# Performance work log

Measured on AMD Instinct MI355X. Metric: run time of the kernel, lower is better.

## Reference

```python
import jax, jax.numpy as jnp
import numpy as np

N = 100_000      # nodes
E = 1_600_000    # edges (avg degree 16)
IN, H, OUT = 960, 192, 3
NB = 6           # block_num


def setup_inputs() -> dict:
    key = jax.random.key(0)
    ks = jax.random.split(key, 14)
    s = 0.05  # weight init scale
    x = jax.random.normal(ks[0], (N, IN), jnp.float32)
    src = jax.random.randint(ks[1], (E,), 0, N, jnp.int32)
    dst = jax.random.randint(ks[2], (E,), 0, N, jnp.int32)
    # normalized adjacency values (like D^-1 A entries)
    ew = jax.random.uniform(ks[3], (E,), jnp.float32) / 16.0
    w1 = jax.random.normal(ks[4], (IN, H), jnp.float32) * s
    l1 = jax.random.normal(ks[5], (IN, H), jnp.float32) * s
    b1 = jnp.zeros((H,), jnp.float32)
    wb = jax.random.normal(ks[6], (2 * NB, H, H), jnp.float32) * s
    lb = jax.random.normal(ks[7], (2 * NB, H, H), jnp.float32) * s
    bb = jnp.zeros((2 * NB, H), jnp.float32)
    w2 = jax.random.normal(ks[8], (H, OUT), jnp.float32) * s
    l2 = jax.random.normal(ks[9], (H, OUT), jnp.float32) * s
    b2 = jnp.zeros((OUT,), jnp.float32)
    return dict(x=x, src=src, dst=dst, ew=ew, w1=w1, l1=l1, b1=b1,
                wb=wb, lb=lb, bb=bb, w2=w2, l2=l2, b2=b2)


def reference(x, src, dst, ew, w1, l1, b1, wb, lb, bb, w2, l2, b2):
    def gcn(h, w, lw, b):
        # GraphConvolution: spmm(adj, h @ w) + h @ loop_w + b
        sup = h @ w                                   # [N, F_out]
        msg = sup[src] * ew[:, None]                  # gather + weight  [E, F_out]
        agg = jax.ops.segment_sum(msg, dst, num_segments=N)
        return agg + h @ lw + b

    h = gcn(x, w1, l1, b1)                            # conv1: in_dim -> hidden
    for i in range(NB):                               # GResBlocks
        a = gcn(h, wb[2 * i], lb[2 * i], bb[2 * i])
        a = gcn(a, wb[2 * i + 1], lb[2 * i + 1], bb[2 * i + 1])
        h = (h + a) * 0.5                             # residual scaling
    x_cat = h
    x_out = gcn(x_cat, w2, l2, b2)                    # conv2: hidden -> out_dim
    return (x_out, x_cat)
```

## Files before the change

kernel.cpp:

```cpp
#include <hip/hip_runtime.h>

typedef __attribute__((ext_vector_type(8))) short short8;
typedef __attribute__((ext_vector_type(4))) float f32x4;
typedef __attribute__((ext_vector_type(4))) int int4v;
typedef __attribute__((ext_vector_type(2))) unsigned int u32x2;

__device__ __forceinline__ float bf2f(unsigned short u) {
  return __uint_as_float(((unsigned)u) << 16);
}
__device__ __forceinline__ unsigned short f2bf(float f) {
  unsigned u = __float_as_uint(f);
  return (unsigned short)((u + 0x7FFFu + ((u >> 16) & 1u)) >> 16);
}

#define GLB_CAST(p) ((const __attribute__((address_space(1))) void*)(p))
#define LDS_CAST(p) ((__attribute__((address_space(3))) void*)(p))

__global__ void count_kernel(const int* __restrict__ dst, int* __restrict__ cnt, int E) {
  int e = blockIdx.x * blockDim.x + threadIdx.x;
  if (e < E) atomicAdd(&cnt[dst[e] + 1], 1);
}

__global__ __launch_bounds__(256) void scan_bsum_kernel(const int* __restrict__ cnt,
                                                        int* __restrict__ bsum, int n) {
  __shared__ int buf[256];
  int tid = threadIdx.x;
  int j0 = blockIdx.x * 1024 + tid * 4;
  int s = 0;
#pragma unroll
  for (int k = 0; k < 4; k++) {
    int j = j0 + k;
    if (j < n) s += cnt[j];
  }
  buf[tid] = s;
  __syncthreads();
  for (int off = 128; off > 0; off >>= 1) {
    if (tid < off) buf[tid] += buf[tid + off];
    __syncthreads();
  }
  if (tid == 0) bsum[blockIdx.x] = buf[0];
}

__global__ __launch_bounds__(256) void scan_small_kernel(const int* __restrict__ bsum,
                                                         int* __restrict__ boff, int nb) {
  __shared__ int buf[2][256];
  int tid = threadIdx.x;
  int C = (nb + 255) >> 8;
  int start = tid * C;
  int end = start + C; if (end > nb) end = nb;
  int s = 0;
  for (int j = start; j < end; j++) s += bsum[j];
  buf[0][tid] = s;
  __syncthreads();
  int pin = 0;
  for (int off = 1; off < 256; off <<= 1) {
    int v = buf[pin][tid];
    if (tid >= off) v += buf[pin][tid - off];
    buf[pin ^ 1][tid] = v;
    pin ^= 1;
    __syncthreads();
  }
  int run = (tid == 0) ? 0 : buf[pin][tid - 1];
  for (int j = start; j < end; j++) {
    boff[j] = run;
    run += bsum[j];
  }
}

__global__ __launch_bounds__(256) void scan_final_kernel(const int* __restrict__ cnt,
                                                         const int* __restrict__ boff,
                                                         int* __restrict__ rowptr,
                                                         int* __restrict__ cur,
                                                         int n, int nrows) {
  __shared__ int buf[2][256];
  int tid = threadIdx.x;
  int j0 = blockIdx.x * 1024 + tid * 4;
  int v[4];
  int s = 0;
#pragma unroll
  for (int k = 0; k < 4; k++) {
    int j = j0 + k;
    v[k] = (j < n) ? cnt[j] : 0;
    s += v[k];
  }
  buf[0][tid] = s;
  __syncthreads();
  int pin = 0;
  for (int off = 1; off < 256; off <<= 1) {
    int t = buf[pin][tid];
    if (tid >= off) t += buf[pin][tid - off];
    buf[pin ^ 1][tid] = t;
    pin ^= 1;
    __syncthreads();
  }
  int run = boff[blockIdx.x] + ((tid == 0) ? 0 : buf[pin][tid - 1]);
#pragma unroll
  for (int k = 0; k < 4; k++) {
    int j = j0 + k;
    if (j < n) {
      run += v[k];
      rowptr[j] = run;
      if (j < nrows) cur[j] = run;
    }
  }
}

__global__ void fill_kernel(const int* __restrict__ src, const int* __restrict__ dst,
                            const float* __restrict__ ew,
                            int* __restrict__ cur, int2* __restrict__ s_edge, int E) {
  int e = blockIdx.x * blockDim.x + threadIdx.x;
  if (e >= E) return;
  int r = dst[e];
  int pos = atomicAdd(&cur[r], 1);
  s_edge[pos] = make_int2(src[e], __float_as_int(ew[e]));
}

__global__ void prep_w_kernel(const float* __restrict__ w1,
                              const float* __restrict__ l1,
                              const float* __restrict__ wb,
                              const float* __restrict__ lb,
                              unsigned short* __restrict__ Wt1,
                              unsigned short* __restrict__ Wcatb) {
  int tid = blockIdx.x * blockDim.x + threadIdx.x;
  const int n1 = 384 * 960;
  const int nc = 12 * 192 * 384;
  if (tid < n1) {
    int c = tid / 960, k = tid % 960;
    Wt1[tid] = f2bf((c < 192) ? w1[k * 192 + c] : l1[k * 192 + (c - 192)]);
  } else if (tid < n1 + nc) {
    int u = tid - n1;
    int i = u / (192 * 384);
    int r = u % (192 * 384);
    int c = r / 384, k = r % 384;
    Wcatb[u] = f2bf((k < 192) ? wb[((size_t)i * 192 + k) * 192 + c]
                              : lb[((size_t)i * 192 + (k - 192)) * 192 + c]);
  }
}

__device__ __forceinline__ short8 cvt_pair(f32x4 a, f32x4 b) {
  short8 r;
  r[0] = (short)f2bf(a[0]); r[1] = (short)f2bf(a[1]);
  r[2] = (short)f2bf(a[2]); r[3] = (short)f2bf(a[3]);
  r[4] = (short)f2bf(b[0]); r[5] = (short)f2bf(b[1]);
  r[6] = (short)f2bf(b[2]); r[7] = (short)f2bf(b[3]);
  return r;
}

__global__ __launch_bounds__(512) void gemm_f32_kernel(const float* __restrict__ A,
                                                       const unsigned short* __restrict__ Wt,
                                                       unsigned short* __restrict__ out,
                                                       int nrows, int K) {
  __shared__ char lds_raw[40960];

  int tid = threadIdx.x;
  int lane = tid & 63;
  int w = tid >> 6;
  int rg = w >> 1, ch = w & 1;
  int row0blk = blockIdx.x * 256;
  int row0 = row0blk + rg * 64;
  int l15 = lane & 15, lq = lane >> 4;

  f32x4 acc[12][4];
#pragma unroll
  for (int cf = 0; cf < 12; cf++)
#pragma unroll
    for (int rf = 0; rf < 4; rf++) acc[cf][rf] = (f32x4)(0.0f);

  int tiles = K / 32;
  for (int tile = 0; tile < tiles; ++tile) {
    __syncthreads();
#pragma unroll
    for (int it = 0; it < 3; ++it) {
      int slot = it * 512 + tid;
      int q = slot / 384, c = slot - q * 384;
      const unsigned short* g = Wt + (size_t)c * K + tile * 32 + q * 8;
      __builtin_amdgcn_global_load_lds(GLB_CAST(g), LDS_CAST(lds_raw + 16384 + slot * 16), 16, 0, 0);
    }
#pragma unroll
    for (int it = 0; it < 2; ++it) {
      int slot = it * 512 + tid;
      int c = slot >> 8, row = slot & 255;
      int grow = row0blk + row;
      if (grow > nrows - 1) grow = nrows - 1;
      const float* g = A + (size_t)grow * K + tile * 32 + c * 8;
      f32x4 a0 = *reinterpret_cast<const f32x4*>(g);
      f32x4 a1 = *reinterpret_cast<const f32x4*>(g + 4);
      *reinterpret_cast<short8*>(lds_raw + slot * 16) = cvt_pair(a0, a1);
    }
    __syncthreads();

    short8 af[4];
#pragma unroll
    for (int rf = 0; rf < 4; rf++)
      af[rf] = *reinterpret_cast<const short8*>(
          lds_raw + lq * 4096 + (rg * 64 + rf * 16 + l15) * 16);
#pragma unroll
    for (int cf = 0; cf < 12; cf++) {
      const short8 bf = *reinterpret_cast<const short8*>(
          lds_raw + 16384 + (lq * 384 + ch * 192 + cf * 16 + l15) * 16);
#pragma unroll
      for (int rf = 0; rf < 4; rf++)
        acc[cf][rf] = __builtin_amdgcn_mfma_f32_16x16x32_bf16(bf, af[rf], acc[cf][rf], 0, 0, 0);
    }
  }

#pragma unroll
  for (int rf = 0; rf < 4; rf++) {
    int row = row0 + rf * 16 + l15;
    if (row >= nrows) continue;
    unsigned short* orow = out + (size_t)row * 384 + ch * 192 + lq * 4;
#pragma unroll
    for (int cf = 0; cf < 12; cf++) {
      u32x2 pv;
      pv[0] = (unsigned)f2bf(acc[cf][rf][0]) | ((unsigned)f2bf(acc[cf][rf][1]) << 16);
      pv[1] = (unsigned)f2bf(acc[cf][rf][2]) | ((unsigned)f2bf(acc[cf][rf][3]) << 16);
      *reinterpret_cast<u32x2*>(orow + cf * 16) = pv;
    }
  }
}

__global__ __launch_bounds__(256) void gemm_cat_kernel(const unsigned short* __restrict__ A1,
                                                       const unsigned short* __restrict__ A2,
                                                       const unsigned short* __restrict__ Wcat,
                                                       const float* __restrict__ bias,
                                                       const unsigned short* __restrict__ hprev,
                                                       unsigned short* __restrict__ out,
                                                       int nrows) {
  __shared__ char lds[28672];

  int tid = threadIdx.x;
  int lane = tid & 63;
  int rg = tid >> 6;
  int row0blk = blockIdx.x * 256;
  int l15 = lane & 15, lq = lane >> 4;

  f32x4 acc[12][4];
#pragma unroll
  for (int cf = 0; cf < 12; cf++)
#pragma unroll
    for (int rf = 0; rf < 4; rf++) acc[cf][rf] = (f32x4)(0.0f);

  for (int tile = 0; tile < 12; ++tile) {
    __syncthreads();
#pragma unroll
    for (int it = 0; it < 3; ++it) {
      int slot = it * 256 + tid;
      int q = slot / 192, c = slot - q * 192;
      const unsigned short* g = Wcat + (size_t)c * 384 + tile * 32 + q * 8;
      __builtin_amdgcn_global_load_lds(GLB_CAST(g), LDS_CAST(lds + 16384 + slot * 16), 16, 0, 0);
    }
    {
      const unsigned short* arr = (tile < 6) ? A1 : A2;
      int koff = (tile < 6 ? tile : tile - 6) * 32;
#pragma unroll
      for (int it = 0; it < 4; ++it) {
        int slot = it * 256 + tid;
        int q = slot >> 8, row = slot & 255;
        int grow = row0blk + row;
        if (grow > nrows - 1) grow = nrows - 1;
        const unsigned short* g = arr + (size_t)grow * 192 + koff + q * 8;
        __builtin_amdgcn_global_load_lds(GLB_CAST(g), LDS_CAST(lds + slot * 16), 16, 0, 0);
      }
    }
    __syncthreads();

    short8 af[4];
#pragma unroll
    for (int rf = 0; rf < 4; rf++)
      af[rf] = *reinterpret_cast<const short8*>(
          lds + (lq * 256 + rg * 64 + rf * 16 + l15) * 16);
#pragma unroll
    for (int cf = 0; cf < 12; cf++) {
      const short8 bf = *reinterpret_cast<const short8*>(
          lds + 16384 + (lq * 192 + cf * 16 + l15) * 16);
#pragma unroll
      for (int rf = 0; rf < 4; rf++)
        acc[cf][rf] = __builtin_amdgcn_mfma_f32_16x16x32_bf16(bf, af[rf], acc[cf][rf], 0, 0, 0);
    }
  }

#pragma unroll
  for (int rf = 0; rf < 4; rf++) {
    int row = row0blk + rg * 64 + rf * 16 + l15;
    if (row >= nrows) continue;
    unsigned short* orow = out + (size_t)row * 192 + lq * 4;
#pragma unroll
    for (int cf = 0; cf < 12; cf++) {
      int col = cf * 16 + lq * 4;
      f32x4 bv = *reinterpret_cast<const f32x4*>(bias + col);
      float r[4];
#pragma unroll
      for (int j = 0; j < 4; j++) r[j] = acc[cf][rf][j] + bv[j];
      if (hprev) {
        u32x2 hp = *reinterpret_cast<const u32x2*>(&hprev[(size_t)row * 192 + col]);
        r[0] = 0.5f * (bf2f((unsigned short)(hp[0] & 0xFFFF)) + r[0]);
        r[1] = 0.5f * (bf2f((unsigned short)(hp[0] >> 16)) + r[1]);
        r[2] = 0.5f * (bf2f((unsigned short)(hp[1] & 0xFFFF)) + r[2]);
        r[3] = 0.5f * (bf2f((unsigned short)(hp[1] >> 16)) + r[3]);
      }
      u32x2 pv;
      pv[0] = (unsigned)f2bf(r[0]) | ((unsigned)f2bf(r[1]) << 16);
      pv[1] = (unsigned)f2bf(r[2]) | ((unsigned)f2bf(r[3]) << 16);
      *reinterpret_cast<u32x2*>(orow + cf * 16) = pv;
    }
  }
}

__global__ __launch_bounds__(256) void spmm_t_kernel(const unsigned short* __restrict__ t,
                                                     const int* __restrict__ rowptr,
                                                     const int2* __restrict__ s_edge,
                                                     const float* __restrict__ bias,
                                                     unsigned short* __restrict__ out16,
                                                     int n) {
  int tid = blockIdx.x * blockDim.x + threadIdx.x;
  int node = tid >> 3;
  int sub = tid & 7;
  if (node >= n) return;
  int co = sub * 8;

  float acc[3][8];
#pragma unroll
  for (int q = 0; q < 3; q++)
#pragma unroll
    for (int j = 0; j < 8; j++) acc[q][j] = 0.0f;

  int e0 = rowptr[node], e1 = rowptr[node + 1];
  int ne = e1 - e0;
  int base = 0;
  for (; base + 8 <= ne; base += 8) {
    int2 rec = s_edge[e0 + base + sub];
#pragma unroll
    for (int half = 0; half < 2; half++) {
      short8 v[4][3];
      float wgt[4];
#pragma unroll
      for (int k = 0; k < 4; k++) {
        int kk = half * 4 + k;
        int sn = __shfl(rec.x, kk, 8);
        wgt[k] = __int_as_float(__shfl(rec.y, kk, 8));
        const unsigned short* row = t + (size_t)sn * 384;
#pragma unroll
        for (int q = 0; q < 3; q++)
          v[k][q] = *reinterpret_cast<const short8*>(row + q * 64 + co);
      }
#pragma unroll
      for (int k = 0; k < 4; k++)
#pragma unroll
        for (int q = 0; q < 3; q++)
#pragma unroll
          for (int j = 0; j < 8; j++)
            acc[q][j] += wgt[k] * bf2f((unsigned short)v[k][q][j]);
    }
  }
  for (; base < ne; base++) {
    int2 rec = s_edge[e0 + base];
    float wgt = __int_as_float(rec.y);
    const unsigned short* row = t + (size_t)rec.x * 384;
#pragma unroll
    for (int q = 0; q < 3; q++) {
      short8 v = *reinterpret_cast<const short8*>(row + q * 64 + co);
#pragma unroll
      for (int j = 0; j < 8; j++) acc[q][j] += wgt * bf2f((unsigned short)v[j]);
    }
  }

  const unsigned short* hlrow = t + (size_t)node * 384 + 192;
#pragma unroll
  for (int q = 0; q < 3; q++) {
    short8 hlv = *reinterpret_cast<const short8*>(hlrow + q * 64 + co);
    unsigned short o16[8];
#pragma unroll
    for (int j = 0; j < 8; j++)
      o16[j] = f2bf(acc[q][j] + bf2f((unsigned short)hlv[j]) + bias[q * 64 + co + j]);
    *reinterpret_cast<int4v*>(&out16[(size_t)node * 192 + q * 64 + co]) =
        *reinterpret_cast<const int4v*>(o16);
  }
}

__global__ __launch_bounds__(256) void spmm_g_kernel(const unsigned short* __restrict__ h,
                                                     const int* __restrict__ rowptr,
                                                     const int2* __restrict__ s_edge,
                                                     unsigned short* __restrict__ g16,
                                                     int n) {
  int tid = blockIdx.x * blockDim.x + threadIdx.x;
  int node = tid >> 3;
  int sub = tid & 7;
  if (node >= n) return;
  int co = sub * 8;

  float acc[3][8];
#pragma unroll
  for (int q = 0; q < 3; q++)
#pragma unroll
    for (int j = 0; j < 8; j++) acc[q][j] = 0.0f;

  int e0 = rowptr[node], e1 = rowptr[node + 1];
  int ne = e1 - e0;
  int base = 0;
  for (; base + 8 <= ne; base += 8) {
    int2 rec = s_edge[e0 + base + sub];
#pragma unroll
    for (int half = 0; half < 2; half++) {
      short8 v[4][3];
      float wgt[4];
#pragma unroll
      for (int k = 0; k < 4; k++) {
        int kk = half * 4 + k;
        int sn = __shfl(rec.x, kk, 8);
        wgt[k] = __int_as_float(__shfl(rec.y, kk, 8));
        const unsigned short* row = h + (size_t)sn * 192;
#pragma unroll
        for (int q = 0; q < 3; q++)
          v[k][q] = *reinterpret_cast<const short8*>(row + q * 64 + co);
      }
#pragma unroll
      for (int k = 0; k < 4; k++)
#pragma unroll
        for (int q = 0; q < 3; q++)
#pragma unroll
          for (int j = 0; j < 8; j++)
            acc[q][j] += wgt[k] * bf2f((unsigned short)v[k][q][j]);
    }
  }
  for (; base < ne; base++) {
    int2 rec = s_edge[e0 + base];
    float wgt = __int_as_float(rec.y);
    const unsigned short* row = h + (size_t)rec.x * 192;
#pragma unroll
    for (int q = 0; q < 3; q++) {
      short8 v = *reinterpret_cast<const short8*>(row + q * 64 + co);
#pragma unroll
      for (int j = 0; j < 8; j++) acc[q][j] += wgt * bf2f((unsigned short)v[j]);
    }
  }

#pragma unroll
  for (int q = 0; q < 3; q++) {
    unsigned short o16[8];
#pragma unroll
    for (int j = 0; j < 8; j++) o16[j] = f2bf(acc[q][j]);
    *reinterpret_cast<int4v*>(&g16[(size_t)node * 192 + q * 64 + co]) =
        *reinterpret_cast<const int4v*>(o16);
  }
}

__global__ __launch_bounds__(256) void cvt_kernel(const unsigned short* __restrict__ h16,
                                                  float* __restrict__ h32, int n8) {
  int i = blockIdx.x * blockDim.x + threadIdx.x;
  if (i >= n8) return;
  short8 v = *reinterpret_cast<const short8*>(&h16[(size_t)i * 8]);
  f32x4 lo, hi;
#pragma unroll
  for (int j = 0; j < 4; j++) {
    lo[j] = bf2f((unsigned short)v[j]);
    hi[j] = bf2f((unsigned short)v[4 + j]);
  }
  *reinterpret_cast<f32x4*>(&h32[(size_t)i * 8]) = lo;
  *reinterpret_cast<f32x4*>(&h32[(size_t)i * 8 + 4]) = hi;
}

__global__ __launch_bounds__(256) void conv2a_kernel(const unsigned short* __restrict__ h,
                                                     const float* __restrict__ w2,
                                                     const float* __restrict__ l2,
                                                     const float* __restrict__ b2,
                                                     float* __restrict__ sup2,
                                                     float* __restrict__ hl2, int n) {
  int wid = (blockIdx.x * blockDim.x + threadIdx.x) >> 6;
  int lane = threadIdx.x & 63;
  if (wid >= n) return;
  float sa[3] = {0.f, 0.f, 0.f}, sl[3] = {0.f, 0.f, 0.f};
  for (int k = lane; k < 192; k += 64) {
    float hv = bf2f(h[(size_t)wid * 192 + k]);
#pragma unroll
    for (int j = 0; j < 3; j++) {
      sa[j] += hv * w2[k * 3 + j];
      sl[j] += hv * l2[k * 3 + j];
    }
  }
#pragma unroll
  for (int j = 0; j < 3; j++) {
    for (int off = 32; off > 0; off >>= 1) {
      sa[j] += __shfl_down(sa[j], off);
      sl[j] += __shfl_down(sl[j], off);
    }
  }
  if (lane == 0) {
#pragma unroll
    for (int j = 0; j < 3; j++) {
      sup2[(size_t)wid * 3 + j] = sa[j];
      hl2[(size_t)wid * 3 + j] = sl[j] + b2[j];
    }
  }
}

__global__ __launch_bounds__(256) void conv2b_kernel(const int* __restrict__ rowptr,
                                                     const int2* __restrict__ s_edge,
                                                     const float* __restrict__ sup2,
                                                     const float* __restrict__ hl2,
                                                     float* __restrict__ out, int n) {
  int node = blockIdx.x * blockDim.x + threadIdx.x;
  if (node >= n) return;
  float acc[3] = {0.f, 0.f, 0.f};
  int e0 = rowptr[node], e1 = rowptr[node + 1];
  for (int e = e0; e < e1; e++) {
    int2 rec = s_edge[e];
    float wgt = __int_as_float(rec.y);
#pragma unroll
    for (int j = 0; j < 3; j++) acc[j] += wgt * sup2[(size_t)rec.x * 3 + j];
  }
#pragma unroll
  for (int j = 0; j < 3; j++)
    out[(size_t)node * 3 + j] = acc[j] + hl2[(size_t)node * 3 + j];
}

extern "C" void kernel_launch(void* const* d_in, const int* in_sizes, int n_in,
                              void* d_out, int out_size, void* d_ws, size_t ws_size,
                              hipStream_t stream) {
  const float* x  = (const float*)d_in[0];
  const int* src  = (const int*)d_in[1];
  const int* dst  = (const int*)d_in[2];
  const float* ew = (const float*)d_in[3];
  const float* w1 = (const float*)d_in[4];
  const float* l1 = (const float*)d_in[5];
  const float* b1 = (const float*)d_in[6];
  const float* wb = (const float*)d_in[7];
  const float* lb = (const float*)d_in[8];
  const float* bb = (const float*)d_in[9];
  const float* w2 = (const float*)d_in[10];
  const float* l2 = (const float*)d_in[11];
  const float* b2 = (const float*)d_in[12];
  float* out = (float*)d_out;

  const int N = in_sizes[0] / 960;
  const int E = in_sizes[1];

  float* h32 = out + (size_t)N * 3;

  char* p = (char*)d_ws;
  auto alloc = [&](size_t bytes) {
    char* q = p;
    p += (bytes + 255) & ~(size_t)255;
    return q;
  };
  unsigned short* Wt1   = (unsigned short*)alloc((size_t)384 * 960 * 2);
  unsigned short* Wcatb = (unsigned short*)alloc((size_t)12 * 192 * 384 * 2);
  unsigned short* t     = (unsigned short*)alloc((size_t)N * 384 * 2);
  unsigned short* h16a  = (unsigned short*)alloc((size_t)N * 192 * 2);
  unsigned short* h16b  = (unsigned short*)alloc((size_t)N * 192 * 2);
  int* rowptr = (int*)alloc((size_t)(N + 1) * 4);
  int* cur    = (int*)alloc((size_t)N * 4);
  int* cnt    = (int*)alloc((size_t)(N + 1) * 4);
  int* bsum   = (int*)alloc((size_t)1024 * 4);
  int* boff   = (int*)alloc((size_t)1024 * 4);
  int2* s_edge = (int2*)alloc((size_t)E * 8);
  float* sup2 = (float*)alloc((size_t)N * 3 * 4);
  float* hl2  = (float*)alloc((size_t)N * 3 * 4);
  if ((size_t)(p - (char*)d_ws) > ws_size) return;

  unsigned short* g16 = t;
  unsigned short* a16 = t + (size_t)N * 192;

  const int nScan = N + 1;
  const int nBlk = (nScan + 1023) / 1024;

  hipMemsetAsync(cnt, 0, (size_t)(N + 1) * 4, stream);
  count_kernel<<<(E + 255) / 256, 256, 0, stream>>>(dst, cnt, E);
  scan_bsum_kernel<<<nBlk, 256, 0, stream>>>(cnt, bsum, nScan);
  scan_small_kernel<<<1, 256, 0, stream>>>(bsum, boff, nBlk);
  scan_final_kernel<<<nBlk, 256, 0, stream>>>(cnt, boff, rowptr, cur, nScan, N);
  fill_kernel<<<(E + 255) / 256, 256, 0, stream>>>(src, dst, ew, cur, s_edge, E);
  {
    int total = 384 * 960 + 12 * 192 * 384;
    prep_w_kernel<<<(total + 255) / 256, 256, 0, stream>>>(w1, l1, wb, lb, Wt1, Wcatb);
  }

  int gBlocks = (N + 255) / 256;
  int sBlocks = (N * 8 + 255) / 256;

  gemm_f32_kernel<<<gBlocks, 512, 0, stream>>>(x, Wt1, t, N, 960);
  spmm_t_kernel<<<sBlocks, 256, 0, stream>>>(t, rowptr, s_edge, b1, h16a, N);

  unsigned short* hcur = h16a;
  unsigned short* hnxt = h16b;
  for (int i = 0; i < 12; i += 2) {
    spmm_g_kernel<<<sBlocks, 256, 0, stream>>>(hcur, rowptr, s_edge, g16, N);
    gemm_cat_kernel<<<gBlocks, 256, 0, stream>>>(
        g16, hcur, Wcatb + (size_t)i * 192 * 384, bb + (size_t)i * 192,
        (const unsigned short*)nullptr, a16, N);
    spmm_g_kernel<<<sBlocks, 256, 0, stream>>>(a16, rowptr, s_edge, g16, N);
    gemm_cat_kernel<<<gBlocks, 256, 0, stream>>>(
        g16, a16, Wcatb + (size_t)(i + 1) * 192 * 384, bb + (size_t)(i + 1) * 192,
        hcur, hnxt, N);
    unsigned short* tmp = hcur; hcur = hnxt; hnxt = tmp;
  }

  cvt_kernel<<<(N * 24 + 255) / 256, 256, 0, stream>>>(hcur, h32, N * 24);

  conv2a_kernel<<<(N + 3) / 4, 256, 0, stream>>>(hcur, w2, l2, b2, sup2, hl2, N);
  conv2b_kernel<<<(N + 255) / 256, 256, 0, stream>>>(rowptr, s_edge, sup2, hl2, out, N);
}
```

Baseline: 2.653 ms.

## Fuse SpMM aggregation into the residual-block GEMM through LDS

Each residual-block GCN layer now runs as one kernel instead of two. The kernel first gathers neighbour rows for 128 nodes and writes the aggregated bf16 tile into LDS. It then runs the concatenated GEMM against the weights, with double-buffered weight and self-feature tiles. This removes the global write and reread of the intermediate g16 buffer and half the launches. In exchange each block uses 72KB of dynamic LDS, has fewer rows per block (128 vs 256), and the weights are reloaded more often.

```diff
diff --git a/kernel.cpp b/kernel.cpp
--- a/kernel.cpp
+++ b/kernel.cpp
@@ -219,78 +219,218 @@
   }
 }
 
-__global__ __launch_bounds__(256) void gemm_cat_kernel(const unsigned short* __restrict__ A1,
-                                                       const unsigned short* __restrict__ A2,
-                                                       const unsigned short* __restrict__ Wcat,
-                                                       const float* __restrict__ bias,
-                                                       const unsigned short* __restrict__ hprev,
-                                                       unsigned short* __restrict__ out,
-                                                       int nrows) {
-  __shared__ char lds[28672];
+__global__ __launch_bounds__(256) void spmm_t_kernel(const unsigned short* __restrict__ t,
+                                                     const int* __restrict__ rowptr,
+                                                     const int2* __restrict__ s_edge,
+                                                     const float* __restrict__ bias,
+                                                     unsigned short* __restrict__ out16,
+                                                     int n) {
+  int tid = blockIdx.x * blockDim.x + threadIdx.x;
+  int node = tid >> 3;
+  int sub = tid & 7;
+  if (node >= n) return;
+  int co = sub * 8;
+
+  float acc[3][8];
+#pragma unroll
+  for (int q = 0; q < 3; q++)
+#pragma unroll
+    for (int j = 0; j < 8; j++) acc[q][j] = 0.0f;
+
+  int e0 = rowptr[node], e1 = rowptr[node + 1];
+  int ne = e1 - e0;
+  int base = 0;
+  for (; base + 8 <= ne; base += 8) {
+    int2 rec = s_edge[e0 + base + sub];
+#pragma unroll
+    for (int half = 0; half < 2; half++) {
+      short8 v[4][3];
+      float wgt[4];
+#pragma unroll
+      for (int k = 0; k < 4; k++) {
+        int kk = half * 4 + k;
+        int sn = __shfl(rec.x, kk, 8);
+        wgt[k] = __int_as_float(__shfl(rec.y, kk, 8));
+        const unsigned short* row = t + (size_t)sn * 384;
+#pragma unroll
+        for (int q = 0; q < 3; q++)
+          v[k][q] = *reinterpret_cast<const short8*>(row + q * 64 + co);
+      }
+#pragma unroll
+      for (int k = 0; k < 4; k++)
+#pragma unroll
+        for (int q = 0; q < 3; q++)
+#pragma unroll
+          for (int j = 0; j < 8; j++)
+            acc[q][j] += wgt[k] * bf2f((unsigned short)v[k][q][j]);
+    }
+  }
+  for (; base < ne; base++) {
+    int2 rec = s_edge[e0 + base];
+    float wgt = __int_as_float(rec.y);
+    const unsigned short* row = t + (size_t)rec.x * 384;
+#pragma unroll
+    for (int q = 0; q < 3; q++) {
+      short8 v = *reinterpret_cast<const short8*>(row + q * 64 + co);
+#pragma unroll
+      for (int j = 0; j < 8; j++) acc[q][j] += wgt * bf2f((unsigned short)v[j]);
+    }
+  }
+
+  const unsigned short* hlrow = t + (size_t)node * 384 + 192;
+#pragma unroll
+  for (int q = 0; q < 3; q++) {
+    short8 hlv = *reinterpret_cast<const short8*>(hlrow + q * 64 + co);
+    unsigned short o16[8];
+#pragma unroll
+    for (int j = 0; j < 8; j++)
+      o16[j] = f2bf(acc[q][j] + bf2f((unsigned short)hlv[j]) + bias[q * 64 + co + j]);
+    *reinterpret_cast<int4v*>(&out16[(size_t)node * 192 + q * 64 + co]) =
+        *reinterpret_cast<const int4v*>(o16);
+  }
+}
+
+__global__ __launch_bounds__(512) void fused_res_kernel(const unsigned short* __restrict__ h,
+                                                        const int* __restrict__ rowptr,
+                                                        const int2* __restrict__ s_edge,
+                                                        const unsigned short* __restrict__ Wcat,
+                                                        const float* __restrict__ bias,
+                                                        const unsigned short* __restrict__ hprev,
+                                                        unsigned short* __restrict__ outp,
+                                                        int n) {
+  extern __shared__ char lds[];
+  const int BOFF = 49152;
 
   int tid = threadIdx.x;
   int lane = tid & 63;
+  int row0 = blockIdx.x * 128;
+
+  {
+    int nloc = tid >> 2;
+    int sub = tid & 3;
+    int grow = row0 + nloc;
+    if (grow > n - 1) grow = n - 1;
+    float acc[6][8];
+#pragma unroll
+    for (int jq = 0; jq < 6; jq++)
+#pragma unroll
+      for (int j = 0; j < 8; j++) acc[jq][j] = 0.0f;
+
+    int e0 = rowptr[grow], e1 = rowptr[grow + 1];
+    int ne = e1 - e0;
+    int base = 0;
+    for (; base + 4 <= ne; base += 4) {
+      int2 rec = s_edge[e0 + base + sub];
+#pragma unroll
+      for (int kp = 0; kp < 2; kp++) {
+        short8 v[2][6];
+        float wg[2];
+#pragma unroll
+        for (int k = 0; k < 2; k++) {
+          int kk = kp * 2 + k;
+          int sn = __shfl(rec.x, kk, 4);
+          wg[k] = __int_as_float(__shfl(rec.y, kk, 4));
+          const unsigned short* rowp = h + (size_t)sn * 192;
+#pragma unroll
+          for (int jq = 0; jq < 6; jq++)
+            v[k][jq] = *reinterpret_cast<const short8*>(rowp + (jq * 4 + sub) * 8);
+        }
+#pragma unroll
+        for (int k = 0; k < 2; k++)
+#pragma unroll
+          for (int jq = 0; jq < 6; jq++)
+#pragma unroll
+            for (int j = 0; j < 8; j++)
+              acc[jq][j] += wg[k] * bf2f((unsigned short)v[k][jq][j]);
+      }
+    }
+    for (; base < ne; base++) {
+      int2 rec = s_edge[e0 + base];
+      float wg = __int_as_float(rec.y);
+      const unsigned short* rowp = h + (size_t)rec.x * 192;
+#pragma unroll
+      for (int jq = 0; jq < 6; jq++) {
+        short8 v = *reinterpret_cast<const short8*>(rowp + (jq * 4 + sub) * 8);
+#pragma unroll
+        for (int j = 0; j < 8; j++) acc[jq][j] += wg * bf2f((unsigned short)v[j]);
+      }
+    }
+#pragma unroll
+    for (int jq = 0; jq < 6; jq++) {
+      int q = jq * 4 + sub;
+      unsigned short o[8];
+#pragma unroll
+      for (int j = 0; j < 8; j++) o[j] = f2bf(acc[jq][j]);
+      *reinterpret_cast<int4v*>(lds + (q * 128 + nloc) * 16) =
+          *reinterpret_cast<const int4v*>(o);
+    }
+  }
+
+  auto stageB = [&](int t, int buf) {
+    {
+      int slot = tid;
+      int q = slot / 192, c = slot - q * 192;
+      const unsigned short* g = Wcat + (size_t)c * 384 + t * 32 + q * 8;
+      __builtin_amdgcn_global_load_lds(GLB_CAST(g),
+                                       LDS_CAST(lds + BOFF + buf * 12288 + slot * 16), 16, 0, 0);
+    }
+    if (tid < 256) {
+      int slot = 512 + tid;
+      int q = slot / 192, c = slot - q * 192;
+      const unsigned short* g = Wcat + (size_t)c * 384 + t * 32 + q * 8;
+      __builtin_amdgcn_global_load_lds(GLB_CAST(g),
+                                       LDS_CAST(lds + BOFF + buf * 12288 + slot * 16), 16, 0, 0);
+    }
+  };
+
+  stageB(0, 0);
+  __syncthreads();
+
   int rg = tid >> 6;
-  int row0blk = blockIdx.x * 256;
   int l15 = lane & 15, lq = lane >> 4;
-
-  f32x4 acc[12][4];
-#pragma unroll
-  for (int cf = 0; cf < 12; cf++)
-#pragma unroll
-    for (int rf = 0; rf < 4; rf++) acc[cf][rf] = (f32x4)(0.0f);
-
-  for (int tile = 0; tile < 12; ++tile) {
-    __syncthreads();
-#pragma unroll
-    for (int it = 0; it < 3; ++it) {
-      int slot = it * 256 + tid;
-      int q = slot / 192, c = slot - q * 192;
-      const unsigned short* g = Wcat + (size_t)c * 384 + tile * 32 + q * 8;
-      __builtin_amdgcn_global_load_lds(GLB_CAST(g), LDS_CAST(lds + 16384 + slot * 16), 16, 0, 0);
-    }
-    {
-      const unsigned short* arr = (tile < 6) ? A1 : A2;
-      int koff = (tile < 6 ? tile : tile - 6) * 32;
-#pragma unroll
-      for (int it = 0; it < 4; ++it) {
-        int slot = it * 256 + tid;
-        int q = slot >> 8, row = slot & 255;
-        int grow = row0blk + row;
-        if (grow > nrows - 1) grow = nrows - 1;
-        const unsigned short* g = arr + (size_t)grow * 192 + koff + q * 8;
-        __builtin_amdgcn_global_load_lds(GLB_CAST(g), LDS_CAST(lds + slot * 16), 16, 0, 0);
+  f32x4 acc[12];
+#pragma unroll
+  for (int cf = 0; cf < 12; cf++) acc[cf] = (f32x4)(0.0f);
+
+  for (int t = 0; t < 12; ++t) {
+    if (t + 1 < 12) {
+      stageB(t + 1, (t + 1) & 1);
+      if (t + 1 >= 6) {
+        int slot = tid;
+        int q = slot >> 7, row = slot & 127;
+        int grow = row0 + row;
+        if (grow > n - 1) grow = n - 1;
+        const unsigned short* g = h + (size_t)grow * 192 + (t + 1 - 6) * 32 + q * 8;
+        __builtin_amdgcn_global_load_lds(GLB_CAST(g),
+                                         LDS_CAST(lds + ((t + 1) & 1) * 8192 + slot * 16), 16, 0, 0);
       }
     }
-    __syncthreads();
-
-    short8 af[4];
-#pragma unroll
-    for (int rf = 0; rf < 4; rf++)
-      af[rf] = *reinterpret_cast<const short8*>(
-          lds + (lq * 256 + rg * 64 + rf * 16 + l15) * 16);
+
+    short8 af;
+    if (t < 6)
+      af = *reinterpret_cast<const short8*>(lds + ((t * 4 + lq) * 128 + rg * 16 + l15) * 16);
+    else
+      af = *reinterpret_cast<const short8*>(lds + (t & 1) * 8192 + (lq * 128 + rg * 16 + l15) * 16);
+
 #pragma unroll
     for (int cf = 0; cf < 12; cf++) {
       const short8 bf = *reinterpret_cast<const short8*>(
-          lds + 16384 + (lq * 192 + cf * 16 + l15) * 16);
-#pragma unroll
-      for (int rf = 0; rf < 4; rf++)
-        acc[cf][rf] = __builtin_amdgcn_mfma_f32_16x16x32_bf16(bf, af[rf], acc[cf][rf], 0, 0, 0);
-    }
-  }
-
-#pragma unroll
-  for (int rf = 0; rf < 4; rf++) {
-    int row = row0blk + rg * 64 + rf * 16 + l15;
-    if (row >= nrows) continue;
-    unsigned short* orow = out + (size_t)row * 192 + lq * 4;
+          lds + BOFF + (t & 1) * 12288 + (lq * 192 + cf * 16 + l15) * 16);
+      acc[cf] = __builtin_amdgcn_mfma_f32_16x16x32_bf16(bf, af, acc[cf], 0, 0, 0);
+    }
+    __syncthreads();
+  }
+
+  int row = row0 + rg * 16 + l15;
+  if (row < n) {
+    unsigned short* orow = outp + (size_t)row * 192 + lq * 4;
 #pragma unroll
     for (int cf = 0; cf < 12; cf++) {
       int col = cf * 16 + lq * 4;
       f32x4 bv = *reinterpret_cast<const f32x4*>(bias + col);
       float r[4];
 #pragma unroll
-      for (int j = 0; j < 4; j++) r[j] = acc[cf][rf][j] + bv[j];
+      for (int j = 0; j < 4; j++) r[j] = acc[cf][j] + bv[j];
       if (hprev) {
         u32x2 hp = *reinterpret_cast<const u32x2*>(&hprev[(size_t)row * 192 + col]);
         r[0] = 0.5f * (bf2f((unsigned short)(hp[0] & 0xFFFF)) + r[0]);
@@ -303,144 +443,6 @@
       pv[1] = (unsigned)f2bf(r[2]) | ((unsigned)f2bf(r[3]) << 16);
       *reinterpret_cast<u32x2*>(orow + cf * 16) = pv;
     }
-  }
-}
-
-__global__ __launch_bounds__(256) void spmm_t_kernel(const unsigned short* __restrict__ t,
-                                                     const int* __restrict__ rowptr,
-                                                     const int2* __restrict__ s_edge,
-                                                     const float* __restrict__ bias,
-                                                     unsigned short* __restrict__ out16,
-                                                     int n) {
-  int tid = blockIdx.x * blockDim.x + threadIdx.x;
-  int node = tid >> 3;
-  int sub = tid & 7;
-  if (node >= n) return;
-  int co = sub * 8;
-
-  float acc[3][8];
-#pragma unroll
-  for (int q = 0; q < 3; q++)
-#pragma unroll
-    for (int j = 0; j < 8; j++) acc[q][j] = 0.0f;
-
-  int e0 = rowptr[node], e1 = rowptr[node + 1];
-  int ne = e1 - e0;
-  int base = 0;
-  for (; base + 8 <= ne; base += 8) {
-    int2 rec = s_edge[e0 + base + sub];
-#pragma unroll
-    for (int half = 0; half < 2; half++) {
-      short8 v[4][3];
-      float wgt[4];
-#pragma unroll
-      for (int k = 0; k < 4; k++) {
-        int kk = half * 4 + k;
-        int sn = __shfl(rec.x, kk, 8);
-        wgt[k] = __int_as_float(__shfl(rec.y, kk, 8));
-        const unsigned short* row = t + (size_t)sn * 384;
-#pragma unroll
-        for (int q = 0; q < 3; q++)
-          v[k][q] = *reinterpret_cast<const short8*>(row + q * 64 + co);
-      }
-#pragma unroll
-      for (int k = 0; k < 4; k++)
-#pragma unroll
-        for (int q = 0; q < 3; q++)
-#pragma unroll
-          for (int j = 0; j < 8; j++)
-            acc[q][j] += wgt[k] * bf2f((unsigned short)v[k][q][j]);
-    }
-  }
-  for (; base < ne; base++) {
-    int2 rec = s_edge[e0 + base];
-    float wgt = __int_as_float(rec.y);
-    const unsigned short* row = t + (size_t)rec.x * 384;
-#pragma unroll
-    for (int q = 0; q < 3; q++) {
-      short8 v = *reinterpret_cast<const short8*>(row + q * 64 + co);
-#pragma unroll
-      for (int j = 0; j < 8; j++) acc[q][j] += wgt * bf2f((unsigned short)v[j]);
-    }
-  }
-
-  const unsigned short* hlrow = t + (size_t)node * 384 + 192;
-#pragma unroll
-  for (int q = 0; q < 3; q++) {
-    short8 hlv = *reinterpret_cast<const short8*>(hlrow + q * 64 + co);
-    unsigned short o16[8];
-#pragma unroll
-    for (int j = 0; j < 8; j++)
-      o16[j] = f2bf(acc[q][j] + bf2f((unsigned short)hlv[j]) + bias[q * 64 + co + j]);
-    *reinterpret_cast<int4v*>(&out16[(size_t)node * 192 + q * 64 + co]) =
-        *reinterpret_cast<const int4v*>(o16);
-  }
-}
-
-__global__ __launch_bounds__(256) void spmm_g_kernel(const unsigned short* __restrict__ h,
-                                                     const int* __restrict__ rowptr,
-                                                     const int2* __restrict__ s_edge,
-                                                     unsigned short* __restrict__ g16,
-                                                     int n) {
-  int tid = blockIdx.x * blockDim.x + threadIdx.x;
-  int node = tid >> 3;
-  int sub = tid & 7;
-  if (node >= n) return;
-  int co = sub * 8;
-
-  float acc[3][8];
-#pragma unroll
-  for (int q = 0; q < 3; q++)
-#pragma unroll
-    for (int j = 0; j < 8; j++) acc[q][j] = 0.0f;
-
-  int e0 = rowptr[node], e1 = rowptr[node + 1];
-  int ne = e1 - e0;
-  int base = 0;
-  for (; base + 8 <= ne; base += 8) {
-    int2 rec = s_edge[e0 + base + sub];
-#pragma unroll
-    for (int half = 0; half < 2; half++) {
-      short8 v[4][3];
-      float wgt[4];
-#pragma unroll
-      for (int k = 0; k < 4; k++) {
-        int kk = half * 4 + k;
-        int sn = __shfl(rec.x, kk, 8);
-        wgt[k] = __int_as_float(__shfl(rec.y, kk, 8));
-        const unsigned short* row = h + (size_t)sn * 192;
-#pragma unroll
-        for (int q = 0; q < 3; q++)
-          v[k][q] = *reinterpret_cast<const short8*>(row + q * 64 + co);
-      }
-#pragma unroll
-      for (int k = 0; k < 4; k++)
-#pragma unroll
-        for (int q = 0; q < 3; q++)
-#pragma unroll
-          for (int j = 0; j < 8; j++)
-            acc[q][j] += wgt[k] * bf2f((unsigned short)v[k][q][j]);
-    }
-  }
-  for (; base < ne; base++) {
-    int2 rec = s_edge[e0 + base];
-    float wgt = __int_as_float(rec.y);
-    const unsigned short* row = h + (size_t)rec.x * 192;
-#pragma unroll
-    for (int q = 0; q < 3; q++) {
-      short8 v = *reinterpret_cast<const short8*>(row + q * 64 + co);
-#pragma unroll
-      for (int j = 0; j < 8; j++) acc[q][j] += wgt * bf2f((unsigned short)v[j]);
-    }
-  }
-
-#pragma unroll
-  for (int q = 0; q < 3; q++) {
-    unsigned short o16[8];
-#pragma unroll
-    for (int j = 0; j < 8; j++) o16[j] = f2bf(acc[q][j]);
-    *reinterpret_cast<int4v*>(&g16[(size_t)node * 192 + q * 64 + co]) =
-        *reinterpret_cast<const int4v*>(o16);
   }
 }
 
@@ -557,8 +559,7 @@
   float* hl2  = (float*)alloc((size_t)N * 3 * 4);
   if ((size_t)(p - (char*)d_ws) > ws_size) return;
 
-  unsigned short* g16 = t;
-  unsigned short* a16 = t + (size_t)N * 192;
+  unsigned short* a16 = t;
 
   const int nScan = N + 1;
   const int nBlk = (nScan + 1023) / 1024;
@@ -576,6 +577,8 @@
 
   int gBlocks = (N + 255) / 256;
   int sBlocks = (N * 8 + 255) / 256;
+  int fBlocks = (N + 127) / 128;
+  const int F_LDS = 73728;
 
   gemm_f32_kernel<<<gBlocks, 512, 0, stream>>>(x, Wt1, t, N, 960);
   spmm_t_kernel<<<sBlocks, 256, 0, stream>>>(t, rowptr, s_edge, b1, h16a, N);
@@ -583,13 +586,11 @@
   unsigned short* hcur = h16a;
   unsigned short* hnxt = h16b;
   for (int i = 0; i < 12; i += 2) {
-    spmm_g_kernel<<<sBlocks, 256, 0, stream>>>(hcur, rowptr, s_edge, g16, N);
-    gemm_cat_kernel<<<gBlocks, 256, 0, stream>>>(
-        g16, hcur, Wcatb + (size_t)i * 192 * 384, bb + (size_t)i * 192,
+    fused_res_kernel<<<fBlocks, 512, F_LDS, stream>>>(
+        hcur, rowptr, s_edge, Wcatb + (size_t)i * 192 * 384, bb + (size_t)i * 192,
         (const unsigned short*)nullptr, a16, N);
-    spmm_g_kernel<<<sBlocks, 256, 0, stream>>>(a16, rowptr, s_edge, g16, N);
-    gemm_cat_kernel<<<gBlocks, 256, 0, stream>>>(
-        g16, a16, Wcatb + (size_t)(i + 1) * 192 * 384, bb + (size_t)(i + 1) * 192,
+    fused_res_kernel<<<fBlocks, 512, F_LDS, stream>>>(
+        a16, rowptr, s_edge, Wcatb + (size_t)(i + 1) * 192 * 384, bb + (size_t)(i + 1) * 192,
         hcur, hnxt, N);
     unsigned short* tmp = hcur; hcur = hnxt; hnxt = tmp;
   }
```

After: 2.501 ms. -5.7%, faster.
